# Optimization experiments

Measured on AMD Instinct MI355X. Metric: run time of the kernel, lower is better.

The kernel has to match this reference:

```python
import jax, jax.numpy as jnp
import numpy as np
from jax import lax

DEPTH = 3
L = 2 ** DEPTH          # n_leaves
N_NODES = 2 ** DEPTH - 1
B, C, H, W = 256, 3, 32, 32
OC = 64
K = 3
OUT_WIDTH = 10
INPUT_WIDTH = C * H * W
FC_IN = OC * H * W // 4


def setup_inputs() -> dict:
    key = jax.random.key(0)
    ks = jax.random.split(key, 9)
    f1 = 1.0 / np.sqrt(INPUT_WIDTH)
    u = lambda k, shape, f: jax.random.uniform(k, shape, jnp.float32, -f, f)
    fcf = 1.0 / np.sqrt(FC_IN)
    return {
        "x": jax.random.normal(ks[0], (B, C, H, W), jnp.float32),
        "node_weights": u(ks[1], (N_NODES, INPUT_WIDTH), f1),
        "node_biases": u(ks[2], (N_NODES, 1), f1),
        "cw1s": u(ks[3], (L, OC, C, K, K), f1),
        "cb1s": u(ks[4], (L, OC), f1),
        "cw2s": u(ks[5], (L, OC, OC, K, K), f1),
        "cb2s": u(ks[6], (L, OC), f1),
        "fc_w": u(ks[7], (OUT_WIDTH, FC_IN), fcf),
        "fc_b": u(ks[8], (OUT_WIDTH,), fcf),
    }


def _soft_mixture(xf, node_weights, node_biases):
    # xf: [B, C*H*W] -> per-sample mixture over leaves [B, L]
    b = xf.shape[0]
    mixture = jnp.ones((b, L), xf.dtype)
    for d in range(DEPTH):  # fixed small structural loop over tree depth
        p0, p1 = 2 ** d - 1, 2 ** (d + 1) - 1
        n = 2 ** d
        logits = xf @ node_weights[p0:p1].T + node_biases[p0:p1].T  # [B, n]
        be = jax.nn.sigmoid(logits)
        mod = jnp.stack([1.0 - be, be], axis=-1).reshape(b, 2 * n, 1)
        mixture = (mixture.reshape(b, 2 * n, L // (2 * n)) * mod).reshape(b, L)
    return mixture


def reference(x, node_weights, node_biases, cw1s, cb1s, cw2s, cb2s, fc_w, fc_b):
    b = x.shape[0]
    xf = x.reshape(b, -1)
    mixture = _soft_mixture(xf, node_weights, node_biases)  # [B, L]

    pad = K // 2  # 'same' padding for odd kernel, stride 1
    # conv1 for all leaves at once: stack leaf kernels along output channels
    w1 = cw1s.reshape(L * OC, C, K, K)
    y = lax.conv_general_dilated(x, w1, (1, 1), [(pad, pad), (pad, pad)])
    y = y + cb1s.reshape(1, L * OC, 1, 1)            # [B, L*OC, H, W]
    y = lax.reduce_window(y, -jnp.inf, lax.max, (1, 1, 2, 2), (1, 1, 2, 2), "VALID")
    y = jax.nn.relu(y)                                # [B, L*OC, H/2, W/2]
    # conv2 as grouped conv (one group per leaf)
    w2 = cw2s.reshape(L * OC, OC, K, K)
    y = lax.conv_general_dilated(y, w2, (1, 1), [(pad, pad), (pad, pad)],
                                 feature_group_count=L)
    y = jax.nn.relu(y + cb2s.reshape(1, L * OC, 1, 1))
    y = y.reshape(b, L, OC, H // 2, W // 2)
    out = jnp.einsum("bl,blchw->bchw", mixture, y)    # mixture-weighted sum over leaves
    flat = out.reshape(b, -1)
    return flat @ fc_w.T + fc_b                       # [B, OUT_WIDTH]
```

## Files before the change

kernel.cpp:

```cpp
#include <hip/hip_runtime.h>
#include <cstdint>
#include <cstddef>

#define B_ 256
#define IW_ 3072
#define L_ 8
#define NN_ 7
#define FCIN_ 16384
#define OUTW_ 10
#define ICST 72
#define YPLANE (324 * ICST)
#define WCH 36864

typedef short short8 __attribute__((ext_vector_type(8)));
typedef float f32x4 __attribute__((ext_vector_type(4)));

__device__ __forceinline__ ushort f2bf(float x) {
    uint u = __float_as_uint(x);
    return (ushort)((u + 0x7fffu + ((u >> 16) & 1u)) >> 16);
}
__device__ __forceinline__ float bf2f(ushort b) { return __uint_as_float(((uint)b) << 16); }

__global__ __launch_bounds__(256) void k_prep(const float* __restrict__ w1, ushort* __restrict__ w1fr,
                                              const float* __restrict__ w2, ushort* __restrict__ w2r,
                                              const float* __restrict__ x, const float* __restrict__ nw,
                                              const float* __restrict__ nb, float* __restrict__ mix) {
    int blk = blockIdx.x;
    if (blk < 64) {
        int i = blk * 256 + threadIdx.x;
        int j    = i & 7;
        int lane = (i >> 3) & 63;
        int mt   = (i >> 9) & 3;
        int l    = i >> 11;
        int fr = lane & 15, fq = lane >> 4;
        int oc = mt * 16 + fr;
        int k = fq * 8 + j;
        float w = (k < 27) ? w1[(size_t)(l * 64 + oc) * 27 + k] : 0.f;
        w1fr[i] = f2bf(w);
        return;
    }
    if (blk < 1216) {
        int i = (blk - 64) * 256 + threadIdx.x;
        int j     = i & 7;
        int lane  = (i >> 3) & 63;
        int mt    = (i >> 9) & 3;
        int tap   = (i >> 11) % 9;
        int icc   = (i / 18432) & 1;
        int l     = i / 36864;
        int fr = lane & 15, fq = lane >> 4;
        int oc = mt * 16 + fr;
        int ic = icc * 32 + fq * 8 + j;
        float w = w2[(((size_t)l * 64 + oc) * 64 + ic) * 9 + tap];
        w2r[i] = f2bf(w);
        return;
    }
    __shared__ float red[4 * NN_];
    __shared__ float bes[NN_];
    int b = blk - 1216, tid = threadIdx.x;
    const float* xb = x + (size_t)b * IW_;
    float p[NN_];
#pragma unroll
    for (int n = 0; n < NN_; ++n) p[n] = 0.f;
    for (int i = tid; i < IW_; i += 256) {
        float xv = xb[i];
#pragma unroll
        for (int n = 0; n < NN_; ++n) p[n] = fmaf(xv, nw[n * IW_ + i], p[n]);
    }
#pragma unroll
    for (int n = 0; n < NN_; ++n) {
        float v = p[n];
        for (int off = 32; off > 0; off >>= 1) v += __shfl_xor(v, off);
        if ((tid & 63) == 0) red[(tid >> 6) * NN_ + n] = v;
    }
    __syncthreads();
    if (tid < NN_) {
        float s = red[tid] + red[NN_ + tid] + red[2 * NN_ + tid] + red[3 * NN_ + tid] + nb[tid];
        bes[tid] = 1.f / (1.f + expf(-s));
    }
    __syncthreads();
    if (tid < L_) {
        int leaf = tid;
        float b0 = bes[0];
        float t0 = ((leaf >> 2) & 1) ? b0 : 1.f - b0;
        float b1v = bes[1 + ((leaf >> 2) & 1)];
        float t1 = ((leaf >> 1) & 1) ? b1v : 1.f - b1v;
        float b2v = bes[3 + ((leaf >> 1) & 3)];
        float t2 = (leaf & 1) ? b2v : 1.f - b2v;
        mix[b * L_ + leaf] = t0 * t1 * t2;
    }
}

__global__ __launch_bounds__(512, 1) void k_fused(const float* __restrict__ x,
                                                  const ushort* __restrict__ w1fr,
                                                  const float* __restrict__ cb1,
                                                  const ushort* __restrict__ w2r,
                                                  const float* __restrict__ cb2, const float* __restrict__ mixw,
                                                  float* __restrict__ out1, int boff) {
    __shared__ __align__(16) ushort smem[YPLANE + WCH];
    ushort* yt = smem;
    ushort* wlds = smem + YPLANE;
    float* xpad = (float*)smem;

    int tid = threadIdx.x;
    int bl = blockIdx.x;
    int b = boff + bl;
    int lane = tid & 63, wid = tid >> 6;
    int fr = lane & 15, fq = lane >> 4;
    int g = wid & 1, ng = wid >> 1;

    for (int i = tid; i < 3 * 34 * 34; i += 512) xpad[i] = 0.f;
    __syncthreads();
    for (int i = tid; i < 3072; i += 512) {
        int ch = i >> 10, rr = (i >> 5) & 31, cc = i & 31;
        xpad[(ch * 34 + rr + 1) * 34 + cc + 1] = x[(size_t)b * IW_ + i];
    }
    __syncthreads();

    short8 Bh[8];
#pragma unroll
    for (int i = 0; i < 8; ++i) {
        int Rg = i >> 2;
        int subrow = (i >> 1) & 1;
        int parity = i & 1;
        int prow = (wid * 2 + Rg) * 2 + subrow;
        int pcol = 2 * fr + parity;
#pragma unroll
        for (int j = 0; j < 8; ++j) {
            int k = fq * 8 + j;
            float xv = 0.f;
            if (k < 27) {
                int ic = k / 9;
                int tap = k - ic * 9;
                int dr = tap / 3, dc = tap - dr * 3;
                xv = xpad[(ic * 34 + prow + dr) * 34 + (pcol + dc)];
            }
            Bh[i][j] = (short)f2bf(xv);
        }
    }
    __syncthreads();
    {
        uint4 z; z.x = z.y = z.z = z.w = 0u;
        for (int i = tid; i < YPLANE / 8; i += 512) ((uint4*)yt)[i] = z;
    }
    __syncthreads();

    f32x4 acc[2][4], oacc[2][4];
#pragma unroll
    for (int m = 0; m < 2; ++m)
#pragma unroll
        for (int rl = 0; rl < 4; ++rl) { acc[m][rl] = (f32x4)0.f; oacc[m][rl] = (f32x4)0.f; }

    for (int l = 0; l < 8; ++l) {
        {
            const char* wsrc = (const char*)(w2r + (size_t)l * WCH);
#pragma unroll
            for (int r = 0; r < 9; ++r) {
                int idx = r * 8 + wid;
                const char* gp = wsrc + idx * 1024 + lane * 16;
                __builtin_amdgcn_global_load_lds(
                    (const __attribute__((address_space(1))) uint*)gp,
                    (__attribute__((address_space(3))) uint*)((char*)wlds + idx * 1024),
                    16, 0, 0);
            }
        }

#pragma unroll
        for (int mtg = 0; mtg < 4; ++mtg) {
            short8 ah = *(const short8*)(w1fr + ((size_t)(l * 4 + mtg) * 64 + lane) * 8);
            f32x4 a1[8];
#pragma unroll
            for (int i = 0; i < 8; ++i) {
                f32x4 t = (f32x4)0.f;
                t = __builtin_amdgcn_mfma_f32_16x16x32_bf16(ah, Bh[i], t, 0, 0, 0);
                a1[i] = t;
            }
            float4 bias4 = *(const float4*)(cb1 + l * 64 + mtg * 16 + fq * 4);
            float bb[4] = {bias4.x, bias4.y, bias4.z, bias4.w};
#pragma unroll
            for (int Rg = 0; Rg < 2; ++Rg) {
                ushort hb[4];
#pragma unroll
                for (int j2 = 0; j2 < 4; ++j2) {
                    float m0 = fmaxf(fmaxf(a1[Rg * 4 + 0][j2], a1[Rg * 4 + 1][j2]),
                                     fmaxf(a1[Rg * 4 + 2][j2], a1[Rg * 4 + 3][j2]));
                    float v = fmaxf(m0 + bb[j2], 0.f);
                    hb[j2] = f2bf(v);
                }
                int pr = 2 * wid + Rg;
                int off = ((pr + 1) * 18 + (fr + 1)) * ICST + mtg * 16 + fq * 4;
                uint2 H;
                H.x = (uint)hb[0] | ((uint)hb[1] << 16);
                H.y = (uint)hb[2] | ((uint)hb[3] << 16);
                *(uint2*)&yt[off] = H;
            }
        }
        __syncthreads();

#pragma unroll
        for (int dc = 0; dc < 3; ++dc) {
#pragma unroll
            for (int icc = 0; icc < 2; ++icc) {
                short8 Ah[2][3];
#pragma unroll
                for (int dr = 0; dr < 3; ++dr) {
                    int tap = dr * 3 + dc;
#pragma unroll
                    for (int m = 0; m < 2; ++m) {
                        int mt = 2 * g + m;
                        Ah[m][dr] = *(const short8*)&wlds[(((icc * 9 + tap) * 4 + mt) * 64 + lane) * 8];
                    }
                }
#pragma unroll
                for (int rr = 0; rr < 6; ++rr) {
                    int off = ((4 * ng + rr) * 18 + (fr + dc)) * ICST + icc * 32 + fq * 8;
                    short8 bh = *(const short8*)(yt + off);
#pragma unroll
                    for (int dr = 0; dr < 3; ++dr) {
                        int rl = rr - dr;
                        if (rl >= 0 && rl < 4) {
#pragma unroll
                            for (int m = 0; m < 2; ++m) {
                                acc[m][rl] = __builtin_amdgcn_mfma_f32_16x16x32_bf16(Ah[m][dr], bh, acc[m][rl], 0, 0, 0);
                            }
                        }
                    }
                }
            }
        }
        {
            float mx = mixw[(size_t)b * 8 + l];
#pragma unroll
            for (int m = 0; m < 2; ++m)
#pragma unroll
                for (int j = 0; j < 4; ++j) {
                    float bias = cb2[l * 64 + (2 * g + m) * 16 + fq * 4 + j];
#pragma unroll
                    for (int rl = 0; rl < 4; ++rl) {
                        float v = fmaxf(acc[m][rl][j] + bias, 0.f);
                        oacc[m][rl][j] = fmaf(mx, v, oacc[m][rl][j]);
                        acc[m][rl][j] = 0.f;
                    }
                }
        }
        __syncthreads();
    }

#pragma unroll
    for (int m = 0; m < 2; ++m)
#pragma unroll
        for (int rl = 0; rl < 4; ++rl)
#pragma unroll
            for (int j = 0; j < 4; ++j) {
                int oc = (2 * g + m) * 16 + fq * 4 + j;
                int pos = (4 * ng + rl) * 16 + fr;
                out1[((size_t)bl * 64 + oc) * 256 + pos] = oacc[m][rl][j];
            }
}

__global__ __launch_bounds__(256) void k_fc(const float* __restrict__ out1, const float* __restrict__ fcw,
                                            const float* __restrict__ fcb, float* __restrict__ out, int boff) {
    __shared__ float red[4][OUTW_];
    int tid = threadIdx.x;
    int bl = blockIdx.x;
    const float4* flat = (const float4*)(out1 + (size_t)bl * FCIN_);
    float pj[OUTW_];
#pragma unroll
    for (int j = 0; j < OUTW_; ++j) pj[j] = 0.f;
    for (int i = tid; i < FCIN_ / 4; i += 256) {
        float4 v = flat[i];
#pragma unroll
        for (int j = 0; j < OUTW_; ++j) {
            float4 w = ((const float4*)(fcw + (size_t)j * FCIN_))[i];
            pj[j] += v.x * w.x + v.y * w.y + v.z * w.z + v.w * w.w;
        }
    }
#pragma unroll
    for (int j = 0; j < OUTW_; ++j) {
        float v = pj[j];
        for (int off = 32; off > 0; off >>= 1) v += __shfl_xor(v, off);
        if ((tid & 63) == 0) red[tid >> 6][j] = v;
    }
    __syncthreads();
    if (tid < OUTW_) {
        float s = red[0][tid] + red[1][tid] + red[2][tid] + red[3][tid] + fcb[tid];
        out[(size_t)(boff + bl) * OUTW_ + tid] = s;
    }
}

extern "C" void kernel_launch(void* const* d_in, const int* in_sizes, int n_in,
                              void* d_out, int out_size, void* d_ws, size_t ws_size,
                              hipStream_t stream) {
    const float* x   = (const float*)d_in[0];
    const float* nw  = (const float*)d_in[1];
    const float* nb  = (const float*)d_in[2];
    const float* w1  = (const float*)d_in[3];
    const float* cb1 = (const float*)d_in[4];
    const float* w2  = (const float*)d_in[5];
    const float* cb2 = (const float*)d_in[6];
    const float* fcw = (const float*)d_in[7];
    const float* fcb = (const float*)d_in[8];
    float* out = (float*)d_out;

    float*  ws   = (float*)d_ws;
    float*  mix  = ws;
    ushort* w1fr = (ushort*)(mix + 2048);
    ushort* w2r  = w1fr + 16384;
    float*  out1 = (float*)(w2r + 294912);

    long avail = (long)ws_size - 630784L;
    int Bc = (int)(avail / 65536L);
    if (Bc > B_) Bc = B_;
    if (Bc < 1) Bc = 1;

    k_prep<<<1472, 256, 0, stream>>>(w1, w1fr, w2, w2r, x, nw, nb, mix);

    for (int boff = 0; boff < B_; boff += Bc) {
        int bc = (B_ - boff < Bc) ? (B_ - boff) : Bc;
        k_fused<<<bc, 512, 0, stream>>>(x, w1fr, cb1, w2r, cb2, mix, out1, boff);
        k_fc<<<bc, 256, 0, stream>>>(out1, fcw, fcb, out, boff);
    }
}
```

Baseline: 81.24 us.

## Fuse final FC layer into conv kernel using pre-transposed FC weights

The separate FC kernel and the out1 intermediate buffer are removed. Each conv block now multiplies its mixture-weighted activations by a transposed, padded FC weight matrix built in the prep kernel, then reduces across waves in shared memory. This drops a global write and re-read of activations plus one launch, and removes the batch chunking loop. The cost is extra prep work and per-thread strided float4 loads of FC weights inside the conv kernel.

```diff
diff --git a/kernel.cpp b/kernel.cpp
--- a/kernel.cpp
+++ b/kernel.cpp
@@ -23,6 +23,7 @@
 
 __global__ __launch_bounds__(256) void k_prep(const float* __restrict__ w1, ushort* __restrict__ w1fr,
                                               const float* __restrict__ w2, ushort* __restrict__ w2r,
+                                              const float* __restrict__ fcw, float* __restrict__ fcwT,
                                               const float* __restrict__ x, const float* __restrict__ nw,
                                               const float* __restrict__ nb, float* __restrict__ mix) {
     int blk = blockIdx.x;
@@ -54,9 +55,15 @@
         w2r[i] = f2bf(w);
         return;
     }
+    if (blk < 1984) {
+        int i = (blk - 1216) * 256 + threadIdx.x;
+        int e = i / 12, j = i - e * 12;
+        fcwT[i] = (j < OUTW_) ? fcw[(size_t)j * FCIN_ + e] : 0.f;
+        return;
+    }
     __shared__ float red[4 * NN_];
     __shared__ float bes[NN_];
-    int b = blk - 1216, tid = threadIdx.x;
+    int b = blk - 1984, tid = threadIdx.x;
     const float* xb = x + (size_t)b * IW_;
     float p[NN_];
 #pragma unroll
@@ -95,7 +102,8 @@
                                                   const float* __restrict__ cb1,
                                                   const ushort* __restrict__ w2r,
                                                   const float* __restrict__ cb2, const float* __restrict__ mixw,
-                                                  float* __restrict__ out1, int boff) {
+                                                  const float* __restrict__ fcwT, const float* __restrict__ fcb,
+                                                  float* __restrict__ out, int boff) {
     __shared__ __align__(16) ushort smem[YPLANE + WCH];
     ushort* yt = smem;
     ushort* wlds = smem + YPLANE;
@@ -245,45 +253,40 @@
         __syncthreads();
     }
 
+    float pj[OUTW_];
+#pragma unroll
+    for (int j = 0; j < OUTW_; ++j) pj[j] = 0.f;
 #pragma unroll
     for (int m = 0; m < 2; ++m)
 #pragma unroll
         for (int rl = 0; rl < 4; ++rl)
 #pragma unroll
-            for (int j = 0; j < 4; ++j) {
-                int oc = (2 * g + m) * 16 + fq * 4 + j;
+            for (int jj = 0; jj < 4; ++jj) {
+                int oc = (2 * g + m) * 16 + fq * 4 + jj;
                 int pos = (4 * ng + rl) * 16 + fr;
-                out1[((size_t)bl * 64 + oc) * 256 + pos] = oacc[m][rl][j];
-            }
-}
-
-__global__ __launch_bounds__(256) void k_fc(const float* __restrict__ out1, const float* __restrict__ fcw,
-                                            const float* __restrict__ fcb, float* __restrict__ out, int boff) {
-    __shared__ float red[4][OUTW_];
-    int tid = threadIdx.x;
-    int bl = blockIdx.x;
-    const float4* flat = (const float4*)(out1 + (size_t)bl * FCIN_);
-    float pj[OUTW_];
-#pragma unroll
-    for (int j = 0; j < OUTW_; ++j) pj[j] = 0.f;
-    for (int i = tid; i < FCIN_ / 4; i += 256) {
-        float4 v = flat[i];
-#pragma unroll
-        for (int j = 0; j < OUTW_; ++j) {
-            float4 w = ((const float4*)(fcw + (size_t)j * FCIN_))[i];
-            pj[j] += v.x * w.x + v.y * w.y + v.z * w.z + v.w * w.w;
-        }
-    }
+                int e = oc * 256 + pos;
+                const float4* fp = (const float4*)(fcwT + (size_t)e * 12);
+                float4 f0 = fp[0], f1 = fp[1], f2 = fp[2];
+                float v = oacc[m][rl][jj];
+                pj[0] = fmaf(v, f0.x, pj[0]); pj[1] = fmaf(v, f0.y, pj[1]);
+                pj[2] = fmaf(v, f0.z, pj[2]); pj[3] = fmaf(v, f0.w, pj[3]);
+                pj[4] = fmaf(v, f1.x, pj[4]); pj[5] = fmaf(v, f1.y, pj[5]);
+                pj[6] = fmaf(v, f1.z, pj[6]); pj[7] = fmaf(v, f1.w, pj[7]);
+                pj[8] = fmaf(v, f2.x, pj[8]); pj[9] = fmaf(v, f2.y, pj[9]);
+            }
+    float* sred = (float*)smem;
 #pragma unroll
     for (int j = 0; j < OUTW_; ++j) {
         float v = pj[j];
         for (int off = 32; off > 0; off >>= 1) v += __shfl_xor(v, off);
-        if ((tid & 63) == 0) red[tid >> 6][j] = v;
+        if (lane == 0) sred[wid * OUTW_ + j] = v;
     }
     __syncthreads();
     if (tid < OUTW_) {
-        float s = red[0][tid] + red[1][tid] + red[2][tid] + red[3][tid] + fcb[tid];
-        out[(size_t)(boff + bl) * OUTW_ + tid] = s;
+        float s = fcb[tid];
+#pragma unroll
+        for (int w = 0; w < 8; ++w) s += sred[w * OUTW_ + tid];
+        out[(size_t)b * OUTW_ + tid] = s;
     }
 }
 
@@ -305,18 +308,8 @@
     float*  mix  = ws;
     ushort* w1fr = (ushort*)(mix + 2048);
     ushort* w2r  = w1fr + 16384;
-    float*  out1 = (float*)(w2r + 294912);
-
-    long avail = (long)ws_size - 630784L;
-    int Bc = (int)(avail / 65536L);
-    if (Bc > B_) Bc = B_;
-    if (Bc < 1) Bc = 1;
-
-    k_prep<<<1472, 256, 0, stream>>>(w1, w1fr, w2, w2r, x, nw, nb, mix);
-
-    for (int boff = 0; boff < B_; boff += Bc) {
-        int bc = (B_ - boff < Bc) ? (B_ - boff) : Bc;
-        k_fused<<<bc, 512, 0, stream>>>(x, w1fr, cb1, w2r, cb2, mix, out1, boff);
-        k_fc<<<bc, 256, 0, stream>>>(out1, fcw, fcb, out, boff);
-    }
+    float*  fcwT = (float*)(w2r + 294912);
+
+    k_prep<<<2240, 256, 0, stream>>>(w1, w1fr, w2, w2r, fcw, fcwT, x, nw, nb, mix);
+    k_fused<<<B_, 512, 0, stream>>>(x, w1fr, cb1, w2r, cb2, mix, fcwT, fcb, out, 0);
 }
```

Result: slower. 109.6 us (+34.9%).

## Double-buffer conv1 output by input-channel half, read conv2 weights from global

Applied to the files above, without the earlier changes.

Splits each leaf's work into two 32-channel halves and double-buffers the pooled conv1 tile in shared memory, so conv1 for the next stage runs before conv2 of the current one and each stage needs only one barrier. The conv2 weight staging into LDS is removed and weights are loaded straight from global/L2 into registers, which frees LDS for the second buffer. The aim is overlapping the conv1 MFMA/pool work with conv2 and cutting barriers. The cost is global-memory latency on the weight fragments, which are no longer staged in shared memory.

```diff
diff --git a/kernel.cpp b/kernel.cpp
--- a/kernel.cpp
+++ b/kernel.cpp
@@ -8,9 +8,8 @@
 #define NN_ 7
 #define FCIN_ 16384
 #define OUTW_ 10
-#define ICST 72
+#define ICST 40
 #define YPLANE (324 * ICST)
-#define WCH 36864
 
 typedef short short8 __attribute__((ext_vector_type(8)));
 typedef float f32x4 __attribute__((ext_vector_type(4)));
@@ -96,9 +95,7 @@
                                                   const ushort* __restrict__ w2r,
                                                   const float* __restrict__ cb2, const float* __restrict__ mixw,
                                                   float* __restrict__ out1, int boff) {
-    __shared__ __align__(16) ushort smem[YPLANE + WCH];
-    ushort* yt = smem;
-    ushort* wlds = smem + YPLANE;
+    __shared__ __align__(16) ushort smem[2 * YPLANE];
     float* xpad = (float*)smem;
 
     int tid = threadIdx.x;
@@ -140,7 +137,7 @@
     __syncthreads();
     {
         uint4 z; z.x = z.y = z.z = z.w = 0u;
-        for (int i = tid; i < YPLANE / 8; i += 512) ((uint4*)yt)[i] = z;
+        for (int i = tid; i < (2 * YPLANE) / 8; i += 512) ((uint4*)smem)[i] = z;
     }
     __syncthreads();
 
@@ -150,22 +147,12 @@
 #pragma unroll
         for (int rl = 0; rl < 4; ++rl) { acc[m][rl] = (f32x4)0.f; oacc[m][rl] = (f32x4)0.f; }
 
-    for (int l = 0; l < 8; ++l) {
-        {
-            const char* wsrc = (const char*)(w2r + (size_t)l * WCH);
-#pragma unroll
-            for (int r = 0; r < 9; ++r) {
-                int idx = r * 8 + wid;
-                const char* gp = wsrc + idx * 1024 + lane * 16;
-                __builtin_amdgcn_global_load_lds(
-                    (const __attribute__((address_space(1))) uint*)gp,
-                    (__attribute__((address_space(3))) uint*)((char*)wlds + idx * 1024),
-                    16, 0, 0);
-            }
-        }
-
-#pragma unroll
-        for (int mtg = 0; mtg < 4; ++mtg) {
+    auto CONV1 = [&](int s) {
+        int l = s >> 1, icc = s & 1;
+        ushort* yt = smem + (size_t)(s & 1) * YPLANE;
+#pragma unroll
+        for (int mt2 = 0; mt2 < 2; ++mt2) {
+            int mtg = icc * 2 + mt2;
             short8 ah = *(const short8*)(w1fr + ((size_t)(l * 4 + mtg) * 64 + lane) * 8);
             f32x4 a1[8];
 #pragma unroll
@@ -187,47 +174,48 @@
                     hb[j2] = f2bf(v);
                 }
                 int pr = 2 * wid + Rg;
-                int off = ((pr + 1) * 18 + (fr + 1)) * ICST + mtg * 16 + fq * 4;
+                int off = ((pr + 1) * 18 + (fr + 1)) * ICST + mt2 * 16 + fq * 4;
                 uint2 H;
                 H.x = (uint)hb[0] | ((uint)hb[1] << 16);
                 H.y = (uint)hb[2] | ((uint)hb[3] << 16);
                 *(uint2*)&yt[off] = H;
             }
         }
-        __syncthreads();
-
+    };
+
+    auto CONV2 = [&](int s) {
+        int l = s >> 1, icc = s & 1;
+        const ushort* yt = smem + (size_t)(s & 1) * YPLANE;
+        const ushort* wbase = w2r + (size_t)(l * 2 + icc) * 18432;
 #pragma unroll
         for (int dc = 0; dc < 3; ++dc) {
-#pragma unroll
-            for (int icc = 0; icc < 2; ++icc) {
-                short8 Ah[2][3];
+            short8 Ah[2][3];
+#pragma unroll
+            for (int dr = 0; dr < 3; ++dr) {
+                int tap = dr * 3 + dc;
+#pragma unroll
+                for (int m = 0; m < 2; ++m) {
+                    int mt = 2 * g + m;
+                    Ah[m][dr] = *(const short8*)(wbase + ((size_t)(tap * 4 + mt) * 64 + lane) * 8);
+                }
+            }
+#pragma unroll
+            for (int rr = 0; rr < 6; ++rr) {
+                int off = ((4 * ng + rr) * 18 + (fr + dc)) * ICST + fq * 8;
+                short8 bh = *(const short8*)(yt + off);
 #pragma unroll
                 for (int dr = 0; dr < 3; ++dr) {
-                    int tap = dr * 3 + dc;
-#pragma unroll
-                    for (int m = 0; m < 2; ++m) {
-                        int mt = 2 * g + m;
-                        Ah[m][dr] = *(const short8*)&wlds[(((icc * 9 + tap) * 4 + mt) * 64 + lane) * 8];
-                    }
-                }
-#pragma unroll
-                for (int rr = 0; rr < 6; ++rr) {
-                    int off = ((4 * ng + rr) * 18 + (fr + dc)) * ICST + icc * 32 + fq * 8;
-                    short8 bh = *(const short8*)(yt + off);
-#pragma unroll
-                    for (int dr = 0; dr < 3; ++dr) {
-                        int rl = rr - dr;
-                        if (rl >= 0 && rl < 4) {
-#pragma unroll
-                            for (int m = 0; m < 2; ++m) {
-                                acc[m][rl] = __builtin_amdgcn_mfma_f32_16x16x32_bf16(Ah[m][dr], bh, acc[m][rl], 0, 0, 0);
-                            }
+                    int rl = rr - dr;
+                    if (rl >= 0 && rl < 4) {
+#pragma unroll
+                        for (int m = 0; m < 2; ++m) {
+                            acc[m][rl] = __builtin_amdgcn_mfma_f32_16x16x32_bf16(Ah[m][dr], bh, acc[m][rl], 0, 0, 0);
                         }
                     }
                 }
             }
         }
-        {
+        if (icc) {
             float mx = mixw[(size_t)b * 8 + l];
 #pragma unroll
             for (int m = 0; m < 2; ++m)
@@ -242,6 +230,13 @@
                     }
                 }
         }
+    };
+
+    CONV1(0);
+    __syncthreads();
+    for (int s = 0; s < 16; ++s) {
+        if (s < 15) CONV1(s + 1);
+        CONV2(s);
         __syncthreads();
     }
 
```

After: 82.38 us. Within noise of the previous version (+1.4%).
